# Optimization experiments

Hardware: AMD Instinct MI355X
Metric: run time of the kernel (lower is better)

## Reference

```python
import jax, jax.numpy as jnp
import numpy as np

# GCN over dependency trees (aryehgigi/gcn-over-pruned-trees), eval mode:
# dropout = identity, rnn=False, dep_dim=0, no_adj=False.
# Per layer l: Ax = adj @ x ; AxW = Linear_l(Ax) + Linear_l(x) (bias counted twice,
# faithful to `self.W[l](Ax) + self.W[l](gcn_inputs)`) ; AxW /= (adj.sum(2)+1) ; relu.

B, L = 128, 256
VOCAB, EMB, POSV, POSD, NERV, NERD, MEM = 50000, 300, 52, 30, 20, 30, 200
IN_DIM = EMB + POSD + NERD  # 360


def setup_inputs() -> dict:
    key = jax.random.key(0)
    ks = jax.random.split(key, 11)
    words = jax.random.randint(ks[0], (B, L), 0, VOCAB)
    pos = jax.random.randint(ks[1], (B, L), 0, POSV)
    ner = jax.random.randint(ks[2], (B, L), 0, NERV)
    adj = (jax.random.uniform(ks[3], (B, L, L)) < 0.05).astype(jnp.float32)
    emb_W = jax.random.normal(ks[4], (VOCAB, EMB), jnp.float32) * 0.1
    pos_W = jax.random.normal(ks[5], (POSV, POSD), jnp.float32) * 0.1
    ner_W = jax.random.normal(ks[6], (NERV, NERD), jnp.float32) * 0.1
    W0 = jax.random.normal(ks[7], (MEM, IN_DIM), jnp.float32) * (1.0 / np.sqrt(IN_DIM))
    b0 = jnp.zeros((MEM,), jnp.float32)
    W1 = jax.random.normal(ks[8], (MEM, MEM), jnp.float32) * (1.0 / np.sqrt(MEM))
    b1 = jnp.zeros((MEM,), jnp.float32)
    return {"words": words, "pos": pos, "ner": ner, "adj": adj,
            "emb_W": emb_W, "pos_W": pos_W, "ner_W": ner_W,
            "W0": W0, "b0": b0, "W1": W1, "b1": b1}


def reference(words, pos, ner, adj, emb_W, pos_W, ner_W, W0, b0, W1, b1):
    # embedding lookups + concat -> [B, L, IN_DIM]
    x = jnp.concatenate([emb_W[words], pos_W[pos], ner_W[ner]], axis=2)
    denom = jnp.sum(adj, axis=2, keepdims=True) + 1.0  # [B, L, 1]
    mask = ((jnp.sum(adj, axis=2) + jnp.sum(adj, axis=1)) == 0)[..., None]  # [B, L, 1]
    for W, b in ((W0, b0), (W1, b1)):
        Ax = jnp.einsum('bij,bjd->bid', adj, x)  # message passing
        # W(Ax) + W(x) == (Ax + x) @ W.T + 2*b  (bias applied twice, as in source)
        h = (jnp.einsum('bld,md->blm', Ax + x, W) + 2.0 * b) / denom
        x = jax.nn.relu(h)
    return (x, mask)
```

## Files before the change

### kernel.cpp

```cpp
#include <hip/hip_runtime.h>
#include <hip/hip_bf16.h>
#include <stdint.h>

typedef __attribute__((ext_vector_type(8))) short short8;
typedef __attribute__((ext_vector_type(4))) float f32x4;

#define NB 128
#define NL 256
#define NROWS 32768
#define IN_DIM 360
#define KP1 384
#define MEM 200
#define NP 256
#define OUT_X (NROWS * MEM)
#define YTP 264
#define BUFSZ 20480
#define YTOFF 40960


__device__ __forceinline__ unsigned short f2b(float f) {
    unsigned u = __builtin_bit_cast(unsigned, f);
    unsigned r = (u + 0x7FFFu + ((u >> 16) & 1u)) >> 16;
    return (unsigned short)r;
}

__device__ __forceinline__ void gl16(const void* g, void* l) {
    __builtin_amdgcn_global_load_lds((const __attribute__((address_space(1))) unsigned*)g,
                                     (__attribute__((address_space(3))) unsigned*)l, 16, 0, 0);
}

__device__ __forceinline__ short8 gather_chunk(int chunk, const float* __restrict__ er,
                                               const float* __restrict__ pr,
                                               const float* __restrict__ nr) {
    float v[8];
    if (chunk < 37) {
        const float* s = er + chunk * 8;
        float4 a = *(const float4*)s;
        float4 b = *(const float4*)(s + 4);
        v[0] = a.x; v[1] = a.y; v[2] = a.z; v[3] = a.w;
        v[4] = b.x; v[5] = b.y; v[6] = b.z; v[7] = b.w;
    } else if (chunk == 37) {
        float4 a = *(const float4*)(er + 296);
        v[0] = a.x; v[1] = a.y; v[2] = a.z; v[3] = a.w;
        v[4] = 0.f; v[5] = 0.f; v[6] = 0.f; v[7] = 0.f;
    } else if (chunk <= 41) {
        int k0 = chunk * 8 - 304;
        #pragma unroll
        for (int i = 0; i < 8; ++i) v[i] = (k0 + i < 30) ? pr[k0 + i] : 0.f;
    } else if (chunk <= 45) {
        int k0 = chunk * 8 - 336;
        #pragma unroll
        for (int i = 0; i < 8; ++i) v[i] = (k0 + i < 30) ? nr[k0 + i] : 0.f;
    } else {
        #pragma unroll
        for (int i = 0; i < 8; ++i) v[i] = 0.f;
    }
    short8 r;
    #pragma unroll
    for (int i = 0; i < 8; ++i) r[i] = (short)f2b(v[i]);
    return r;
}

__global__ void prep_weights(const float* __restrict__ W0, const float* __restrict__ W1,
                             short* __restrict__ W0p, short* __restrict__ W1p,
                             unsigned* __restrict__ colnz) {
    int idx = blockIdx.x * 256 + threadIdx.x;
    if (idx < NROWS) colnz[idx] = 0u;
    if (idx < NP * KP1) {
        int n = idx / KP1, kp = idx - n * KP1;
        float v = 0.f;
        if (n < MEM) {
            if (kp < 300)                   v = W0[n * IN_DIM + kp];
            else if (kp >= 304 && kp < 334) v = W0[n * IN_DIM + 300 + (kp - 304)];
            else if (kp >= 336 && kp < 366) v = W0[n * IN_DIM + 330 + (kp - 336)];
        }
        W0p[idx] = (short)f2b(v);
    } else {
        int i2 = idx - NP * KP1;
        if (i2 < NP * NP) {
            int n = i2 >> 8, k = i2 & 255;
            float v = (n < MEM && k < MEM) ? W1[n * MEM + k] : 0.f;
            W1p[i2] = (short)f2b(v);
        }
    }
}

__global__ void adjrow_kernel(const float* __restrict__ adj, float* __restrict__ dinv,
                              float* __restrict__ rsum, unsigned short* __restrict__ Sbf,
                              unsigned* __restrict__ colnz) {
    int row = blockIdx.x * 4 + (threadIdx.x >> 6);
    int lane = threadIdx.x & 63;
    const float4* ar = (const float4*)(adj + (size_t)row * NL);
    float4 v = ar[lane];
    float s = v.x + v.y + v.z + v.w;
    #pragma unroll
    for (int off = 32; off >= 1; off >>= 1) s += __shfl_xor(s, off);
    int rloc = row & 255;
    float d0 = v.x + ((lane * 4 + 0) == rloc ? 1.f : 0.f);
    float d1 = v.y + ((lane * 4 + 1) == rloc ? 1.f : 0.f);
    float d2 = v.z + ((lane * 4 + 2) == rloc ? 1.f : 0.f);
    float d3 = v.w + ((lane * 4 + 3) == rloc ? 1.f : 0.f);
    ushort4 st; st.x = f2b(d0); st.y = f2b(d1); st.z = f2b(d2); st.w = f2b(d3);
    *(ushort4*)(Sbf + (size_t)row * NL + lane * 4) = st;
    if (lane == 0) { rsum[row] = s; dinv[row] = 1.0f / (s + 1.0f); }
    unsigned* cz = colnz + ((row >> 8) << 8);
    if (v.x != 0.f) atomicOr(&cz[lane * 4 + 0], 1u);
    if (v.y != 0.f) atomicOr(&cz[lane * 4 + 1], 1u);
    if (v.z != 0.f) atomicOr(&cz[lane * 4 + 2], 1u);
    if (v.w != 0.f) atomicOr(&cz[lane * 4 + 3], 1u);
}

template <int FINAL>
__global__ __launch_bounds__(512, 4) void fused_kernel(
    const short* __restrict__ A, int lda, int nkt,
    const short* __restrict__ Bp, int ldb,
    const unsigned short* __restrict__ Sbf,
    const float* __restrict__ dinv, const float* __restrict__ bias,
    const int* __restrict__ words, const int* __restrict__ pos, const int* __restrict__ ner,
    const float* __restrict__ embW, const float* __restrict__ posW,
    const float* __restrict__ nerW,
    const float* __restrict__ rsum, const unsigned* __restrict__ colnz,
    float* __restrict__ maskout,
    short* __restrict__ x1b, float* __restrict__ outx) {
    extern __shared__ char smem[];
    unsigned short* Yt = (unsigned short*)(smem + YTOFF);

    int bi = blockIdx.x;
    int batch = bi & 127, sl = bi >> 7;

    int tid = threadIdx.x;
    int lane = tid & 63, wid = tid >> 6;
    int wr = wid >> 1, wc = wid & 1;
    int lr = lane & 15, lc = lane >> 4;

    if (FINAL == 0 && sl == 0 && tid < 256) {
        int r = batch * NL + tid;
        maskout[r] = (rsum[r] == 0.f && colnz[r] == 0u) ? 1.0f : 0.0f;
    }

    const short* Bb = Bp + (size_t)sl * 64 * ldb;
    const short* Sb = (const short*)(Sbf + (size_t)batch * NL * NL);

    int r0s = tid >> 2, c0s = tid & 3;
    int r1s = r0s + 128;
    int offA0 = r0s * 64 + (c0s ^ ((r0s >> 1) & 3)) * 16;
    int offA1 = r1s * 64 + (c0s ^ ((r1s >> 1) & 3)) * 16;
    const short* Sp0 = Sb + (size_t)r0s * NL + c0s * 8;
    const short* Sp1 = Sb + (size_t)r1s * NL + c0s * 8;
    int offB = 0; const short* Bpp = nullptr;
    if (tid < 256) {
        int br = tid >> 2, bc = tid & 3;
        offB = 16384 + br * 64 + (bc ^ ((br >> 1) & 3)) * 16;
        Bpp = Bb + (size_t)br * ldb + bc * 8;
    }

    const float *er0 = nullptr, *pr0 = nullptr, *nr0 = nullptr;
    const float *er1 = nullptr, *pr1 = nullptr, *nr1 = nullptr;
    {
        int g0 = batch * NL + r0s, g1 = g0 + 128;
        er0 = embW + (size_t)words[g0] * 300;
        pr0 = posW + (size_t)pos[g0] * 30;
        nr0 = nerW + (size_t)ner[g0] * 30;
        er1 = embW + (size_t)words[g1] * 300;
        pr1 = posW + (size_t)pos[g1] * 30;
        nr1 = nerW + (size_t)ner[g1] * 30;
    }
    #define LOADA(kt, o0, o1) do {                                  \
        int ch_ = (kt) * 4 + c0s;                                   \
        (o0) = gather_chunk(ch_, er0, pr0, nr0);                    \
        (o1) = gather_chunk(ch_, er1, pr1, nr1);                    \
    } while (0)

    f32x4 acc[4][2] = {};
    short8 aR0, aR1, bR;
    LOADA(0, aR0, aR1);
    if (tid < 256) bR = *(const short8*)Bpp;
    *(short8*)(smem + offA0) = aR0;
    *(short8*)(smem + offA1) = aR1;
    if (tid < 256) *(short8*)(smem + offB) = bR;
    LOADA(1, aR0, aR1);
    if (tid < 256) bR = *(const short8*)(Bpp + 32);
    __syncthreads();

    short8 sA0, sA1, sB0, sB1;
    for (int kt = 0; kt < nkt; ++kt) {
        char* base_ = smem + (kt & 1) * BUFSZ;
        short8 af[4], bf[2];
        #pragma unroll
        for (int mi = 0; mi < 4; ++mi) {
            int row = wr * 64 + mi * 16 + lr;
            int cs = lc ^ ((row >> 1) & 3);
            af[mi] = *(const short8*)(base_ + row * 64 + cs * 16);
        }
        #pragma unroll
        for (int ni = 0; ni < 2; ++ni) {
            int row = wc * 32 + ni * 16 + lr;
            int cs = lc ^ ((row >> 1) & 3);
            bf[ni] = *(const short8*)(base_ + 16384 + row * 64 + cs * 16);
        }
        if (kt + 1 < nkt) {
            char* nb_ = smem + ((kt + 1) & 1) * BUFSZ;
            *(short8*)(nb_ + offA0) = aR0;
            *(short8*)(nb_ + offA1) = aR1;
            if (tid < 256) *(short8*)(nb_ + offB) = bR;
        }
        if (kt + 2 < nkt) {
            LOADA(kt + 2, aR0, aR1);
            if (tid < 256) bR = *(const short8*)(Bpp + (kt + 2) * 32);
        } else if (kt + 2 == nkt) {
            sA0 = *(const short8*)Sp0;
            sA1 = *(const short8*)Sp1;
        } else if (kt + 2 == nkt + 1) {
            sB0 = *(const short8*)(Sp0 + 32);
            sB1 = *(const short8*)(Sp1 + 32);
        }
        #pragma unroll
        for (int mi = 0; mi < 4; ++mi)
            #pragma unroll
            for (int ni = 0; ni < 2; ++ni)
                acc[mi][ni] = __builtin_amdgcn_mfma_f32_16x16x32_bf16(af[mi], bf[ni], acc[mi][ni], 0, 0, 0);
        __syncthreads();
    }
    #undef LOADA

    #pragma unroll
    for (int mi = 0; mi < 4; ++mi)
        #pragma unroll
        for (int ni = 0; ni < 2; ++ni) {
            f32x4 v = acc[mi][ni];
            ushort4 st; st.x = f2b(v[0]); st.y = f2b(v[1]); st.z = f2b(v[2]); st.w = f2b(v[3]);
            int col = wc * 32 + ni * 16 + lr;
            int row0 = wr * 64 + mi * 16 + lc * 4;
            *(ushort4*)(Yt + (size_t)col * YTP + row0) = st;
        }
    *(short8*)(smem + offA0) = sA0;
    *(short8*)(smem + offA1) = sA1;
    sA0 = *(const short8*)(Sp0 + 64);
    sA1 = *(const short8*)(Sp1 + 64);
    __syncthreads();

    f32x4 acc2[4][2] = {};
    #pragma unroll
    for (int kt = 0; kt < 8; ++kt) {
        char* base_ = smem + (kt & 1) * BUFSZ;
        short8 ay[4], bs[2];
        #pragma unroll
        for (int mi = 0; mi < 4; ++mi)
            ay[mi] = *(const short8*)(Yt + (size_t)(mi * 16 + lr) * YTP + kt * 32 + lc * 8);
        #pragma unroll
        for (int ni = 0; ni < 2; ++ni) {
            int row = wid * 32 + ni * 16 + lr;
            int cs = lc ^ ((row >> 1) & 3);
            bs[ni] = *(const short8*)(base_ + row * 64 + cs * 16);
        }
        if (kt + 1 < 8) {
            char* nb_ = smem + ((kt + 1) & 1) * BUFSZ;
            if ((kt & 1) == 0) {
                *(short8*)(nb_ + offA0) = sB0;
                *(short8*)(nb_ + offA1) = sB1;
                if (kt + 3 < 8) {
                    sB0 = *(const short8*)(Sp0 + (kt + 3) * 32);
                    sB1 = *(const short8*)(Sp1 + (kt + 3) * 32);
                }
            } else {
                *(short8*)(nb_ + offA0) = sA0;
                *(short8*)(nb_ + offA1) = sA1;
                if (kt + 3 < 8) {
                    sA0 = *(const short8*)(Sp0 + (kt + 3) * 32);
                    sA1 = *(const short8*)(Sp1 + (kt + 3) * 32);
                }
            }
        }
        #pragma unroll
        for (int mi = 0; mi < 4; ++mi)
            #pragma unroll
            for (int ni = 0; ni < 2; ++ni)
                acc2[mi][ni] = __builtin_amdgcn_mfma_f32_16x16x32_bf16(ay[mi], bs[ni], acc2[mi][ni], 0, 0, 0);
        if (kt + 1 < 8) __syncthreads();
    }

    #pragma unroll
    for (int ni = 0; ni < 2; ++ni) {
        int g = batch * NL + wid * 32 + ni * 16 + lr;
        float di = dinv[g];
        #pragma unroll
        for (int mi = 0; mi < 4; ++mi) {
            int col0 = sl * 64 + mi * 16 + lc * 4;
            float4 bv;
            if (col0 < MEM) bv = *(const float4*)(bias + col0);
            else { bv.x = 0.f; bv.y = 0.f; bv.z = 0.f; bv.w = 0.f; }
            f32x4 z = acc2[mi][ni];
            float h0 = fmaxf((z[0] + 2.f * bv.x) * di, 0.f);
            float h1 = fmaxf((z[1] + 2.f * bv.y) * di, 0.f);
            float h2 = fmaxf((z[2] + 2.f * bv.z) * di, 0.f);
            float h3 = fmaxf((z[3] + 2.f * bv.w) * di, 0.f);
            ushort4 st; st.x = f2b(h0); st.y = f2b(h1); st.z = f2b(h2); st.w = f2b(h3);
            *(ushort4*)((unsigned short*)x1b + (size_t)g * NP + col0) = st;
        }
    }
}

__global__ __launch_bounds__(512, 4) void fused1_kernel(
    const short* __restrict__ A,
    const short* __restrict__ Bp,
    const unsigned short* __restrict__ Sbf,
    const float* __restrict__ dinv, const float* __restrict__ bias,
    float* __restrict__ outx) {
    extern __shared__ char smem[];
    unsigned short* Yt = (unsigned short*)(smem + YTOFF);

    int bi = blockIdx.x;
    int batch = bi & 127, sl = bi >> 7;
    int tid = threadIdx.x;
    int lane = tid & 63, wid = tid >> 6;
    int wr = wid >> 1, wc = wid & 1;
    int lr = lane & 15, lc = lane >> 4;

    const short* Ab = A + (size_t)batch * NL * NP;
    const short* Bb = Bp + (size_t)sl * 64 * NP;
    const short* Sb = (const short*)(Sbf + (size_t)batch * NL * NL);

    int li0 = tid, li1 = tid + 512;
    int rA0 = li0 >> 2, cA0 = (li0 & 3) ^ ((rA0 >> 1) & 3);
    int rA1 = li1 >> 2, cA1 = (li1 & 3) ^ ((rA1 >> 1) & 3);
    const short* srcA0 = Ab + (size_t)rA0 * NP + cA0 * 8;
    const short* srcA1 = Ab + (size_t)rA1 * NP + cA1 * 8;
    const short* srcS0 = Sb + (size_t)rA0 * NL + cA0 * 8;
    const short* srcS1 = Sb + (size_t)rA1 * NL + cA1 * 8;
    const short* srcB = nullptr;
    if (wid < 4) {
        int rB = tid >> 2, cB = (tid & 3) ^ ((rB >> 1) & 3);
        srcB = Bb + (size_t)rB * NP + cB * 8;
    }
    int dA0 = (wid * 64) * 16;
    int dA1 = (512 + wid * 64) * 16;
    int dB  = 16384 + (wid * 64) * 16;

    #define STAGE1(b, kt) do {                                       \
        char* bb_ = smem + (b) * BUFSZ;                              \
        gl16(srcA0 + (kt) * 32, bb_ + dA0);                          \
        gl16(srcA1 + (kt) * 32, bb_ + dA1);                          \
        if (wid < 4) gl16(srcB + (kt) * 32, bb_ + dB);               \
    } while (0)
    #define STAGES(b, kt) do {                                       \
        char* bb_ = smem + (b) * BUFSZ;                              \
        gl16(srcS0 + (kt) * 32, bb_ + dA0);                          \
        gl16(srcS1 + (kt) * 32, bb_ + dA1);                         \
    } while (0)
    #define WAITBAR() do {                                           \
        asm volatile("s_waitcnt vmcnt(0)" ::: "memory");             \
        __builtin_amdgcn_sched_barrier(0);                           \
        __builtin_amdgcn_s_barrier();                                \
    } while (0)

    f32x4 acc[4][2] = {};
    STAGE1(0, 0);
    WAITBAR();
    #pragma unroll
    for (int kt = 0; kt < 8; ++kt) {
        if (kt + 1 < 8) STAGE1((kt + 1) & 1, kt + 1);
        char* base_ = smem + (kt & 1) * BUFSZ;
        short8 af[4], bf[2];
        #pragma unroll
        for (int mi = 0; mi < 4; ++mi) {
            int row = wr * 64 + mi * 16 + lr;
            int cs = lc ^ ((row >> 1) & 3);
            af[mi] = *(const short8*)(base_ + row * 64 + cs * 16);
        }
        #pragma unroll
        for (int ni = 0; ni < 2; ++ni) {
            int row = wc * 32 + ni * 16 + lr;
            int cs = lc ^ ((row >> 1) & 3);
            bf[ni] = *(const short8*)(base_ + 16384 + row * 64 + cs * 16);
        }
        #pragma unroll
        for (int mi = 0; mi < 4; ++mi)
            #pragma unroll
            for (int ni = 0; ni < 2; ++ni)
                acc[mi][ni] = __builtin_amdgcn_mfma_f32_16x16x32_bf16(af[mi], bf[ni], acc[mi][ni], 0, 0, 0);
        WAITBAR();
    }

    STAGES(0, 0);
    #pragma unroll
    for (int mi = 0; mi < 4; ++mi)
        #pragma unroll
        for (int ni = 0; ni < 2; ++ni) {
            f32x4 v = acc[mi][ni];
            ushort4 st; st.x = f2b(v[0]); st.y = f2b(v[1]); st.z = f2b(v[2]); st.w = f2b(v[3]);
            int col = wc * 32 + ni * 16 + lr;
            int row0 = wr * 64 + mi * 16 + lc * 4;
            *(ushort4*)(Yt + (size_t)col * YTP + row0) = st;
        }
    asm volatile("s_waitcnt vmcnt(0)" ::: "memory");
    __builtin_amdgcn_sched_barrier(0);
    __syncthreads();

    f32x4 acc2[4][2] = {};
    #pragma unroll
    for (int kt = 0; kt < 8; ++kt) {
        if (kt + 1 < 8) STAGES((kt + 1) & 1, kt + 1);
        char* base_ = smem + (kt & 1) * BUFSZ;
        short8 ay[4], bs[2];
        #pragma unroll
        for (int mi = 0; mi < 4; ++mi)
            ay[mi] = *(const short8*)(Yt + (size_t)(mi * 16 + lr) * YTP + kt * 32 + lc * 8);
        #pragma unroll
        for (int ni = 0; ni < 2; ++ni) {
            int row = wid * 32 + ni * 16 + lr;
            int cs = lc ^ ((row >> 1) & 3);
            bs[ni] = *(const short8*)(base_ + row * 64 + cs * 16);
        }
        #pragma unroll
        for (int mi = 0; mi < 4; ++mi)
            #pragma unroll
            for (int ni = 0; ni < 2; ++ni)
                acc2[mi][ni] = __builtin_amdgcn_mfma_f32_16x16x32_bf16(ay[mi], bs[ni], acc2[mi][ni], 0, 0, 0);
        if (kt + 1 < 8) WAITBAR();
    }
    #undef STAGE1
    #undef STAGES
    #undef WAITBAR

    #pragma unroll
    for (int ni = 0; ni < 2; ++ni) {
        int g = batch * NL + wid * 32 + ni * 16 + lr;
        float di = dinv[g];
        #pragma unroll
        for (int mi = 0; mi < 4; ++mi) {
            int col0 = sl * 64 + mi * 16 + lc * 4;
            if (col0 < MEM) {
                float4 bv = *(const float4*)(bias + col0);
                f32x4 z = acc2[mi][ni];
                float4 o;
                o.x = fmaxf((z[0] + 2.f * bv.x) * di, 0.f);
                o.y = fmaxf((z[1] + 2.f * bv.y) * di, 0.f);
                o.z = fmaxf((z[2] + 2.f * bv.z) * di, 0.f);
                o.w = fmaxf((z[3] + 2.f * bv.w) * di, 0.f);
                *(float4*)(outx + (size_t)g * MEM + col0) = o;
            }
        }
    }
}

extern "C" void kernel_launch(void* const* d_in, const int* in_sizes, int n_in,
                              void* d_out, int out_size, void* d_ws, size_t ws_size,
                              hipStream_t stream) {
    const int*   words = (const int*)d_in[0];
    const int*   pos   = (const int*)d_in[1];
    const int*   ner   = (const int*)d_in[2];
    const float* adj   = (const float*)d_in[3];
    const float* embW  = (const float*)d_in[4];
    const float* posW  = (const float*)d_in[5];
    const float* nerW  = (const float*)d_in[6];
    const float* W0    = (const float*)d_in[7];
    const float* b0    = (const float*)d_in[8];
    const float* W1    = (const float*)d_in[9];
    const float* b1    = (const float*)d_in[10];
    float* out = (float*)d_out;

    char* ws = (char*)d_ws;
    size_t off = 0;
    short* W0p = (short*)(ws + off);        off += (size_t)NP * KP1 * 2;
    short* W1p = (short*)(ws + off);        off += (size_t)NP * NP * 2;
    short* X1b = (short*)(ws + off);        off += (size_t)NROWS * NP * 2;
    float* dinv = (float*)(ws + off);       off += (size_t)NROWS * 4;
    float* rsum = (float*)(ws + off);       off += (size_t)NROWS * 4;
    unsigned* colnz = (unsigned*)(ws + off); off += (size_t)NROWS * 4;
    unsigned short* Sbf = (unsigned short*)(ws + off); off += (size_t)NROWS * NL * 2;

    prep_weights<<<(NP * KP1 + NP * NP + 255) / 256, 256, 0, stream>>>(W0, W1, W0p, W1p, colnz);
    adjrow_kernel<<<NROWS / 4, 256, 0, stream>>>(adj, dinv, rsum, Sbf, colnz);

    const int ldsB = YTOFF + 64 * YTP * 2;
    fused_kernel<0><<<NB * 4, 512, ldsB, stream>>>(nullptr, KP1, KP1 / 32, W0p, KP1,
                                                   Sbf, dinv, b0,
                                                   words, pos, ner, embW, posW, nerW,
                                                   rsum, colnz, out + OUT_X,
                                                   X1b, nullptr);
    fused1_kernel<<<NB * 4, 512, ldsB, stream>>>(X1b, W1p, Sbf, dinv, b1, out);
}
```

Measured before the change: 81.29 us.

## Fuse adjacency preprocessing into first GCN layer kernel

Removes the separate adjrow kernel and the colnz clearing. The first-layer fused kernel now reads its batch's adjacency itself. It computes row sums and column-nonzero bits with LDS atomics, writes the bf16 adj+I matrix, emits the mask and dinv, and keeps dinv in LDS for the epilogue. This saves a launch, the global atomics and the rsum/colnz buffers. In exchange, each of the four column-slice blocks per batch re-reads the full fp32 adjacency and redundantly rewrites the same Sbf data, raising memory traffic.

```diff
diff --git a/kernel.cpp b/kernel.cpp
--- a/kernel.cpp
+++ b/kernel.cpp
@@ -16,6 +16,7 @@
 #define YTP 264
 #define BUFSZ 20480
 #define YTOFF 40960
+#define RSOFF 74752
 
 
 __device__ __forceinline__ unsigned short f2b(float f) {
@@ -62,10 +63,8 @@
 }
 
 __global__ void prep_weights(const float* __restrict__ W0, const float* __restrict__ W1,
-                             short* __restrict__ W0p, short* __restrict__ W1p,
-                             unsigned* __restrict__ colnz) {
+                             short* __restrict__ W0p, short* __restrict__ W1p) {
     int idx = blockIdx.x * 256 + threadIdx.x;
-    if (idx < NROWS) colnz[idx] = 0u;
     if (idx < NP * KP1) {
         int n = idx / KP1, kp = idx - n * KP1;
         float v = 0.f;
@@ -85,60 +84,80 @@
     }
 }
 
-__global__ void adjrow_kernel(const float* __restrict__ adj, float* __restrict__ dinv,
-                              float* __restrict__ rsum, unsigned short* __restrict__ Sbf,
-                              unsigned* __restrict__ colnz) {
-    int row = blockIdx.x * 4 + (threadIdx.x >> 6);
-    int lane = threadIdx.x & 63;
-    const float4* ar = (const float4*)(adj + (size_t)row * NL);
-    float4 v = ar[lane];
-    float s = v.x + v.y + v.z + v.w;
-    #pragma unroll
-    for (int off = 32; off >= 1; off >>= 1) s += __shfl_xor(s, off);
-    int rloc = row & 255;
-    float d0 = v.x + ((lane * 4 + 0) == rloc ? 1.f : 0.f);
-    float d1 = v.y + ((lane * 4 + 1) == rloc ? 1.f : 0.f);
-    float d2 = v.z + ((lane * 4 + 2) == rloc ? 1.f : 0.f);
-    float d3 = v.w + ((lane * 4 + 3) == rloc ? 1.f : 0.f);
-    ushort4 st; st.x = f2b(d0); st.y = f2b(d1); st.z = f2b(d2); st.w = f2b(d3);
-    *(ushort4*)(Sbf + (size_t)row * NL + lane * 4) = st;
-    if (lane == 0) { rsum[row] = s; dinv[row] = 1.0f / (s + 1.0f); }
-    unsigned* cz = colnz + ((row >> 8) << 8);
-    if (v.x != 0.f) atomicOr(&cz[lane * 4 + 0], 1u);
-    if (v.y != 0.f) atomicOr(&cz[lane * 4 + 1], 1u);
-    if (v.z != 0.f) atomicOr(&cz[lane * 4 + 2], 1u);
-    if (v.w != 0.f) atomicOr(&cz[lane * 4 + 3], 1u);
-}
-
-template <int FINAL>
-__global__ __launch_bounds__(512, 4) void fused_kernel(
-    const short* __restrict__ A, int lda, int nkt,
-    const short* __restrict__ Bp, int ldb,
-    const unsigned short* __restrict__ Sbf,
-    const float* __restrict__ dinv, const float* __restrict__ bias,
+__global__ __launch_bounds__(512, 4) void fused0_kernel(
+    const short* __restrict__ Bp,
+    unsigned short* __restrict__ Sbf,
+    const float* __restrict__ bias,
     const int* __restrict__ words, const int* __restrict__ pos, const int* __restrict__ ner,
     const float* __restrict__ embW, const float* __restrict__ posW,
     const float* __restrict__ nerW,
-    const float* __restrict__ rsum, const unsigned* __restrict__ colnz,
-    float* __restrict__ maskout,
-    short* __restrict__ x1b, float* __restrict__ outx) {
+    const float* __restrict__ adj,
+    float* __restrict__ maskout, float* __restrict__ dinvg,
+    short* __restrict__ x1b) {
     extern __shared__ char smem[];
     unsigned short* Yt = (unsigned short*)(smem + YTOFF);
+    float* dinvL = (float*)(smem + RSOFF);
+    unsigned* colnzL = (unsigned*)(smem + RSOFF + 1024);
 
     int bi = blockIdx.x;
     int batch = bi & 127, sl = bi >> 7;
-
     int tid = threadIdx.x;
     int lane = tid & 63, wid = tid >> 6;
     int wr = wid >> 1, wc = wid & 1;
     int lr = lane & 15, lc = lane >> 4;
 
-    if (FINAL == 0 && sl == 0 && tid < 256) {
-        int r = batch * NL + tid;
-        maskout[r] = (rsum[r] == 0.f && colnz[r] == 0u) ? 1.0f : 0.0f;
-    }
-
-    const short* Bb = Bp + (size_t)sl * 64 * ldb;
+    if (tid < 256) dinvL[tid] = 0.f;
+    if (tid < 8) colnzL[tid] = 0u;
+    __syncthreads();
+    {
+        const float* adjb = adj + (size_t)batch * NL * NL;
+        unsigned short* Sw = Sbf + (size_t)batch * NL * NL;
+        #pragma unroll 4
+        for (int j = 0; j < 16; ++j) {
+            int cidx = j * 512 + tid;
+            int r = cidx >> 5, c0 = (cidx & 31) << 3;
+            const float* src = adjb + (size_t)r * NL + c0;
+            float4 a = *(const float4*)src;
+            float4 b = *(const float4*)(src + 4);
+            float s8 = a.x + a.y + a.z + a.w + b.x + b.y + b.z + b.w;
+            unsigned bits = 0;
+            bits |= (a.x != 0.f) ? 1u : 0u;   bits |= (a.y != 0.f) ? 2u : 0u;
+            bits |= (a.z != 0.f) ? 4u : 0u;   bits |= (a.w != 0.f) ? 8u : 0u;
+            bits |= (b.x != 0.f) ? 16u : 0u;  bits |= (b.y != 0.f) ? 32u : 0u;
+            bits |= (b.z != 0.f) ? 64u : 0u;  bits |= (b.w != 0.f) ? 128u : 0u;
+            #pragma unroll
+            for (int o = 16; o >= 1; o >>= 1) s8 += __shfl_xor(s8, o);
+            if ((lane & 31) == 0) atomicAdd(&dinvL[r], s8);
+            if (bits) atomicOr(&colnzL[c0 >> 5], bits << (c0 & 31));
+            float d0 = a.x + ((c0 + 0 == r) ? 1.f : 0.f);
+            float d1 = a.y + ((c0 + 1 == r) ? 1.f : 0.f);
+            float d2 = a.z + ((c0 + 2 == r) ? 1.f : 0.f);
+            float d3 = a.w + ((c0 + 3 == r) ? 1.f : 0.f);
+            float d4 = b.x + ((c0 + 4 == r) ? 1.f : 0.f);
+            float d5 = b.y + ((c0 + 5 == r) ? 1.f : 0.f);
+            float d6 = b.z + ((c0 + 6 == r) ? 1.f : 0.f);
+            float d7 = b.w + ((c0 + 7 == r) ? 1.f : 0.f);
+            short8 st;
+            st[0] = (short)f2b(d0); st[1] = (short)f2b(d1);
+            st[2] = (short)f2b(d2); st[3] = (short)f2b(d3);
+            st[4] = (short)f2b(d4); st[5] = (short)f2b(d5);
+            st[6] = (short)f2b(d6); st[7] = (short)f2b(d7);
+            *(short8*)(Sw + (size_t)r * NL + c0) = st;
+        }
+    }
+    __syncthreads();
+    if (tid < 256) {
+        float s = dinvL[tid];
+        float di = 1.0f / (s + 1.0f);
+        dinvL[tid] = di;
+        if (sl == 0) {
+            unsigned bit = (colnzL[tid >> 5] >> (tid & 31)) & 1u;
+            maskout[batch * NL + tid] = (s == 0.f && bit == 0u) ? 1.0f : 0.0f;
+            dinvg[batch * NL + tid] = di;
+        }
+    }
+
+    const short* Bb = Bp + (size_t)sl * 64 * KP1;
     const short* Sb = (const short*)(Sbf + (size_t)batch * NL * NL);
 
     int r0s = tid >> 2, c0s = tid & 3;
@@ -151,11 +170,10 @@
     if (tid < 256) {
         int br = tid >> 2, bc = tid & 3;
         offB = 16384 + br * 64 + (bc ^ ((br >> 1) & 3)) * 16;
-        Bpp = Bb + (size_t)br * ldb + bc * 8;
-    }
-
-    const float *er0 = nullptr, *pr0 = nullptr, *nr0 = nullptr;
-    const float *er1 = nullptr, *pr1 = nullptr, *nr1 = nullptr;
+        Bpp = Bb + (size_t)br * KP1 + bc * 8;
+    }
+
+    const float *er0, *pr0, *nr0, *er1, *pr1, *nr1;
     {
         int g0 = batch * NL + r0s, g1 = g0 + 128;
         er0 = embW + (size_t)words[g0] * 300;
@@ -183,6 +201,7 @@
     __syncthreads();
 
     short8 sA0, sA1, sB0, sB1;
+    const int nkt = KP1 / 32;
     for (int kt = 0; kt < nkt; ++kt) {
         char* base_ = smem + (kt & 1) * BUFSZ;
         short8 af[4], bf[2];
@@ -281,8 +300,9 @@
 
     #pragma unroll
     for (int ni = 0; ni < 2; ++ni) {
-        int g = batch * NL + wid * 32 + ni * 16 + lr;
-        float di = dinv[g];
+        int rloc = wid * 32 + ni * 16 + lr;
+        int g = batch * NL + rloc;
+        float di = dinvL[rloc];
         #pragma unroll
         for (int mi = 0; mi < 4; ++mi) {
             int col0 = sl * 64 + mi * 16 + lc * 4;
@@ -290,11 +310,11 @@
             if (col0 < MEM) bv = *(const float4*)(bias + col0);
             else { bv.x = 0.f; bv.y = 0.f; bv.z = 0.f; bv.w = 0.f; }
             f32x4 z = acc2[mi][ni];
-            float h0 = fmaxf((z[0] + 2.f * bv.x) * di, 0.f);
-            float h1 = fmaxf((z[1] + 2.f * bv.y) * di, 0.f);
-            float h2 = fmaxf((z[2] + 2.f * bv.z) * di, 0.f);
-            float h3 = fmaxf((z[3] + 2.f * bv.w) * di, 0.f);
-            ushort4 st; st.x = f2b(h0); st.y = f2b(h1); st.z = f2b(h2); st.w = f2b(h3);
+            ushort4 st;
+            st.x = f2b(fmaxf((z[0] + 2.f * bv.x) * di, 0.f));
+            st.y = f2b(fmaxf((z[1] + 2.f * bv.y) * di, 0.f));
+            st.z = f2b(fmaxf((z[2] + 2.f * bv.z) * di, 0.f));
+            st.w = f2b(fmaxf((z[3] + 2.f * bv.w) * di, 0.f));
             *(ushort4*)((unsigned short*)x1b + (size_t)g * NP + col0) = st;
         }
     }
@@ -345,7 +365,7 @@
     #define STAGES(b, kt) do {                                       \
         char* bb_ = smem + (b) * BUFSZ;                              \
         gl16(srcS0 + (kt) * 32, bb_ + dA0);                          \
-        gl16(srcS1 + (kt) * 32, bb_ + dA1);                         \
+        gl16(srcS1 + (kt) * 32, bb_ + dA1);                          \
     } while (0)
     #define WAITBAR() do {                                           \
         asm volatile("s_waitcnt vmcnt(0)" ::: "memory");             \
@@ -465,18 +485,14 @@
     short* W1p = (short*)(ws + off);        off += (size_t)NP * NP * 2;
     short* X1b = (short*)(ws + off);        off += (size_t)NROWS * NP * 2;
     float* dinv = (float*)(ws + off);       off += (size_t)NROWS * 4;
-    float* rsum = (float*)(ws + off);       off += (size_t)NROWS * 4;
-    unsigned* colnz = (unsigned*)(ws + off); off += (size_t)NROWS * 4;
     unsigned short* Sbf = (unsigned short*)(ws + off); off += (size_t)NROWS * NL * 2;
 
-    prep_weights<<<(NP * KP1 + NP * NP + 255) / 256, 256, 0, stream>>>(W0, W1, W0p, W1p, colnz);
-    adjrow_kernel<<<NROWS / 4, 256, 0, stream>>>(adj, dinv, rsum, Sbf, colnz);
-
-    const int ldsB = YTOFF + 64 * YTP * 2;
-    fused_kernel<0><<<NB * 4, 512, ldsB, stream>>>(nullptr, KP1, KP1 / 32, W0p, KP1,
-                                                   Sbf, dinv, b0,
-                                                   words, pos, ner, embW, posW, nerW,
-                                                   rsum, colnz, out + OUT_X,
-                                                   X1b, nullptr);
-    fused1_kernel<<<NB * 4, 512, ldsB, stream>>>(X1b, W1p, Sbf, dinv, b1, out);
-}
+    prep_weights<<<(NP * KP1 + NP * NP + 255) / 256, 256, 0, stream>>>(W0, W1, W0p, W1p);
+
+    const int ldsB0 = RSOFF + 1024 + 32;
+    const int ldsB1 = YTOFF + 64 * YTP * 2;
+    fused0_kernel<<<NB * 4, 512, ldsB0, stream>>>(W0p, Sbf, b0,
+                                                  words, pos, ner, embW, posW, nerW,
+                                                  adj, out + OUT_X, dinv, X1b);
+    fused1_kernel<<<NB * 4, 512, ldsB1, stream>>>(X1b, W1p, Sbf, dinv, b1, out);
+}
```

Measured after the change: 67.55 us (median of 3 runs). 1.2x faster.
